# Kernel optimization log

Measured on AMD Instinct MI355X. Metric: run time of the kernel, lower is better.

Reference implementation:

```python
import jax, jax.numpy as jnp
import numpy as np

N_NODES = 50000
N_EDGES = 1600000
N_HEAD = 4
F_OUT = 128


def setup_inputs() -> dict:
    key = jax.random.key(0)
    k1, k2, k3, k4 = jax.random.split(key, 4)
    x = jax.random.normal(k1, (N_NODES, F_OUT), dtype=jnp.float32)
    # diag weight [H,1,F]; small scale like xavier on a diag-ish param
    w = jax.random.normal(k2, (N_HEAD, 1, F_OUT), dtype=jnp.float32) * 0.1
    # a_src_dst init: uniform(-stdv, stdv), stdv = 1/sqrt(2*f_out)
    stdv = 1.0 / np.sqrt(2 * F_OUT)
    a = jax.random.uniform(k3, (N_HEAD, 2 * F_OUT, 1), dtype=jnp.float32, minval=-stdv, maxval=stdv)
    edge_index = jax.random.randint(k4, (2, N_EDGES), 0, N_NODES, dtype=jnp.int64)
    return {"x": x, "w": w, "a": a, "edge_index": edge_index}


def reference(x, w, a, edge_index):
    # x: [N,F], w: [H,1,F] (diag), a: [H,2F,1], edge_index: [2,E]
    H, F = w.shape[0], w.shape[-1]
    N = x.shape[0]
    src = edge_index[0]  # row indices (aggregation targets)
    dst = edge_index[1]
    h = x[None, :, :] * w  # [H,N,F]  (diag: elementwise scale per head)
    # split cat(h_src,h_dst)@a into two per-node projections (same math as concat+matmul)
    a_src = a[:, :F, 0]  # [H,F]
    a_dst = a[:, F:, 0]  # [H,F]
    s_src = jnp.einsum('hnf,hf->hn', h, a_src)  # [H,N]
    s_dst = jnp.einsum('hnf,hf->hn', h, a_dst)  # [H,N]
    score = s_src[:, src] + s_dst[:, dst]  # [H,E]
    edge_e = jnp.exp(-jax.nn.leaky_relu(score, negative_slope=0.2))  # [H,E]
    outs = []
    for i in range(H):  # small fixed head loop keeps peak memory at one head's messages
        rowsum = jax.ops.segment_sum(edge_e[i], src, num_segments=N)  # [N]
        msg = edge_e[i][:, None] * h[i][dst]  # [E,F]
        agg = jax.ops.segment_sum(msg, src, num_segments=N)  # [N,F]
        outs.append(agg / rowsum[:, None])
    return jnp.stack(outs, axis=0)  # [H,N,F]
```

## Files before the change

kernel.cpp:

```cpp
#include <hip/hip_runtime.h>

#define N_NODES 50000
#define N_EDGES 1600000
#define N_HEAD 4
#define F_OUT 128
#define CAP 96
#define NPS 512
#define K1 98
#define SCAP 17408
#define NPG 32
#define GROUPS 1563
#define EPB 2048
#define P1_BLOCKS ((N_EDGES + EPB - 1) / EPB)
#define SCORE_BLOCKS ((N_NODES * 64 + 255) / 256)
#define FUSED_BLOCKS (P1_BLOCKS + SCORE_BLOCKS)

__global__ void __launch_bounds__(256) prep_kernel(
    const float* __restrict__ x, const float* __restrict__ w,
    const float* __restrict__ a, float4* __restrict__ s_src4,
    float4* __restrict__ s_dst4,
    const int* __restrict__ src, const int* __restrict__ dst,
    int* __restrict__ gc, unsigned int* __restrict__ region) {
  __shared__ int hist[K1], cur[K1], lstart[K1], gpos[K1];
  __shared__ unsigned int staging[EPB];
  const int tid = threadIdx.x;

  if (blockIdx.x >= P1_BLOCKS) {
    int bid = blockIdx.x - P1_BLOCKS;
    if (bid == 0 && tid == 0) {
      s_dst4[N_NODES] = make_float4(INFINITY, INFINITY, INFINITY, INFINITY);
    }
    int wv = (bid * 256 + tid) >> 6;
    int lane = tid & 63;
    if (wv >= N_NODES) return;
    float xv0 = x[wv * F_OUT + lane];
    float xv1 = x[wv * F_OUT + 64 + lane];
    float ps[N_HEAD], pd[N_HEAD];
#pragma unroll
    for (int h = 0; h < N_HEAD; ++h) {
      float w0 = w[h * F_OUT + lane];
      float w1 = w[h * F_OUT + 64 + lane];
      float as0 = a[h * 2 * F_OUT + lane];
      float as1 = a[h * 2 * F_OUT + 64 + lane];
      float ad0 = a[h * 2 * F_OUT + F_OUT + lane];
      float ad1 = a[h * 2 * F_OUT + F_OUT + 64 + lane];
      ps[h] = xv0 * w0 * as0 + xv1 * w1 * as1;
      pd[h] = xv0 * w0 * ad0 + xv1 * w1 * ad1;
    }
#pragma unroll
    for (int off = 32; off > 0; off >>= 1) {
#pragma unroll
      for (int h = 0; h < N_HEAD; ++h) {
        ps[h] += __shfl_xor(ps[h], off, 64);
        pd[h] += __shfl_xor(pd[h], off, 64);
      }
    }
    if (lane == 0) {
      s_src4[wv] = make_float4(ps[0], ps[1], ps[2], ps[3]);
      s_dst4[wv] = make_float4(pd[0], pd[1], pd[2], pd[3]);
    }
    return;
  }

  const int base = blockIdx.x * EPB;
  int vc = N_EDGES - base;
  if (vc > EPB) vc = EPB;

  unsigned int pk[EPB / 256];
#pragma unroll
  for (int k = 0; k < EPB / 256; ++k) {
    int i = k * 256 + tid;
    if (i < vc) {
      unsigned int s = (unsigned int)src[base + i];
      unsigned int d = (unsigned int)dst[base + i];
      pk[k] = (s << 16) | d;
    } else {
      pk[k] = 0xffffffffu;
    }
  }
  if (tid < K1) { hist[tid] = 0; cur[tid] = 0; }
  __syncthreads();
#pragma unroll
  for (int k = 0; k < EPB / 256; ++k)
    if (pk[k] != 0xffffffffu) atomicAdd(&hist[pk[k] >> 25], 1);
  __syncthreads();
  if (tid < 64) {
    int carry = 0;
    for (int b0 = 0; b0 < K1; b0 += 64) {
      int idx = b0 + tid;
      int h = (idx < K1) ? hist[idx] : 0;
      int v = h;
#pragma unroll
      for (int off = 1; off < 64; off <<= 1) {
        int t = __shfl_up(v, off, 64);
        if (tid >= off) v += t;
      }
      if (idx < K1) {
        lstart[idx] = carry + v - h;
        gpos[idx] = atomicAdd(&gc[idx], h);
      }
      carry += __shfl(v, 63, 64);
    }
  }
  __syncthreads();
#pragma unroll
  for (int k = 0; k < EPB / 256; ++k) {
    if (pk[k] != 0xffffffffu) {
      int b = pk[k] >> 25;
      int pos = lstart[b] + atomicAdd(&cur[b], 1);
      staging[pos] = pk[k];
    }
  }
  __syncthreads();
  for (int i = tid; i < vc; i += 256) {
    unsigned int v = staging[i];
    int b = v >> 25;
    int off = gpos[b] + (i - lstart[b]);
    if (off < SCAP) region[(size_t)b * SCAP + off] = v;
  }
}


#define SCAN_PROC(v)                                                       \
  {                                                                        \
    unsigned int s_ = (v) >> 16;                                           \
    if ((s_ >> 5) == gtag) {                                               \
      int l_ = s_ & 31;                                                    \
      int p_ = atomicAdd(&ncnt[l_], 1);                                    \
      if (p_ < CAP) nbkt[l_][p_] = (int)((v) & 0xffffu);                   \
    }                                                                      \
  }

__global__ void __launch_bounds__(256, 6) agg_kernel(
    const float* __restrict__ x, const float* __restrict__ w,
    const float4* __restrict__ s_src4, const float4* __restrict__ s_dst4,
    const int* __restrict__ gc, const unsigned int* __restrict__ region,
    float* __restrict__ out) {
  __shared__ int ncnt[NPG];
  __shared__ int nbkt[NPG][CAP];
  const int tid = threadIdx.x;
  const int g = blockIdx.x;
  const int sb = g >> 4;
  int c = gc[sb];
  if (c > SCAP) c = SCAP;
  if (tid < NPG) ncnt[tid] = 0;
  __syncthreads();

  const unsigned int* reg = region + (size_t)sb * SCAP;
  const unsigned int gtag = (unsigned int)g;
  {
    const uint4* reg4 = (const uint4*)reg;
    int c4 = c >> 2;
    for (int i = tid; i < c4; i += 256) {
      uint4 v = reg4[i];
      SCAN_PROC(v.x); SCAN_PROC(v.y); SCAN_PROC(v.z); SCAN_PROC(v.w);
    }
    for (int i = (c4 << 2) + tid; i < c; i += 256) {
      unsigned int v = reg[i];
      SCAN_PROC(v);
    }
  }
  __syncthreads();

  const int ws = tid >> 6, lane = tid & 63;
  const int half = lane >> 5;
  const int sl = lane & 31;
  const float4* x4 = (const float4*)x;

  const float4* w4 = (const float4*)w;
  const float4 wA = w4[(half ? 1 : 0) * 32 + sl];
  const float4 wB = w4[(half ? 3 : 2) * 32 + sl];

  float4 ss = s_src4[g * NPG + ws];

  for (int l = ws; l < NPG; l += 4) {
    int n = g * NPG + l;
    if (n >= N_NODES) break;
    int nn = n + 4;
    if (nn > N_NODES - 1) nn = N_NODES - 1;
    float4 ss_next = s_src4[nn];

    int m = ncnt[l];
    m = (m < CAP) ? m : CAP;
    int m_pad = (m + 7) & ~7;
    if (lane < m_pad - m) nbkt[l][m + lane] = N_NODES;

    float4 acc0 = {0.f, 0.f, 0.f, 0.f}, acc1 = {0.f, 0.f, 0.f, 0.f};
    float4 acc2 = {0.f, 0.f, 0.f, 0.f}, acc3 = {0.f, 0.f, 0.f, 0.f};
    float p0 = 0.f, p1 = 0.f, p2 = 0.f, p3 = 0.f;

    for (int t = 0; t < m_pad; t += 8) {
      int dd[4];
      float4 sd[4], xv[4];
#pragma unroll
      for (int q = 0; q < 4; ++q) dd[q] = nbkt[l][t + 2 * q + half];
#pragma unroll
      for (int q = 0; q < 4; ++q) sd[q] = s_dst4[dd[q]];
#pragma unroll
      for (int q = 0; q < 4; ++q) {
        int dx = dd[q] < N_NODES - 1 ? dd[q] : N_NODES - 1;
        xv[q] = x4[(size_t)dx * 32 + sl];
      }
#pragma unroll
      for (int q = 0; q < 4; ++q) {
        float s0 = ss.x + sd[q].x, s1 = ss.y + sd[q].y;
        float s2 = ss.z + sd[q].z, s3 = ss.w + sd[q].w;
        float e0 = __expf(-fmaxf(s0, 0.2f * s0));
        float e1 = __expf(-fmaxf(s1, 0.2f * s1));
        float e2 = __expf(-fmaxf(s2, 0.2f * s2));
        float e3 = __expf(-fmaxf(s3, 0.2f * s3));
        p0 += e0; p1 += e1; p2 += e2; p3 += e3;
        acc0.x = fmaf(e0, xv[q].x, acc0.x); acc0.y = fmaf(e0, xv[q].y, acc0.y);
        acc0.z = fmaf(e0, xv[q].z, acc0.z); acc0.w = fmaf(e0, xv[q].w, acc0.w);
        acc1.x = fmaf(e1, xv[q].x, acc1.x); acc1.y = fmaf(e1, xv[q].y, acc1.y);
        acc1.z = fmaf(e1, xv[q].z, acc1.z); acc1.w = fmaf(e1, xv[q].w, acc1.w);
        acc2.x = fmaf(e2, xv[q].x, acc2.x); acc2.y = fmaf(e2, xv[q].y, acc2.y);
        acc2.z = fmaf(e2, xv[q].z, acc2.z); acc2.w = fmaf(e2, xv[q].w, acc2.w);
        acc3.x = fmaf(e3, xv[q].x, acc3.x); acc3.y = fmaf(e3, xv[q].y, acc3.y);
        acc3.z = fmaf(e3, xv[q].z, acc3.z); acc3.w = fmaf(e3, xv[q].w, acc3.w);
      }
    }

    p0 += __shfl_xor(p0, 32, 64);
    p1 += __shfl_xor(p1, 32, 64);
    p2 += __shfl_xor(p2, 32, 64);
    p3 += __shfl_xor(p3, 32, 64);

    acc0.x += __shfl_xor(acc0.x, 32, 64); acc0.y += __shfl_xor(acc0.y, 32, 64);
    acc0.z += __shfl_xor(acc0.z, 32, 64); acc0.w += __shfl_xor(acc0.w, 32, 64);
    acc1.x += __shfl_xor(acc1.x, 32, 64); acc1.y += __shfl_xor(acc1.y, 32, 64);
    acc1.z += __shfl_xor(acc1.z, 32, 64); acc1.w += __shfl_xor(acc1.w, 32, 64);
    acc2.x += __shfl_xor(acc2.x, 32, 64); acc2.y += __shfl_xor(acc2.y, 32, 64);
    acc2.z += __shfl_xor(acc2.z, 32, 64); acc2.w += __shfl_xor(acc2.w, 32, 64);
    acc3.x += __shfl_xor(acc3.x, 32, 64); acc3.y += __shfl_xor(acc3.y, 32, 64);
    acc3.z += __shfl_xor(acc3.z, 32, 64); acc3.w += __shfl_xor(acc3.w, 32, 64);

    float r0 = 1.f / p0, r1 = 1.f / p1, r2 = 1.f / p2, r3 = 1.f / p3;

    float4 aA = half ? acc1 : acc0;
    float4 aB = half ? acc3 : acc2;
    float rA = half ? r1 : r0;
    float rB = half ? r3 : r2;
    float4 o;
    o.x = wA.x * aA.x * rA; o.y = wA.y * aA.y * rA;
    o.z = wA.z * aA.z * rA; o.w = wA.w * aA.w * rA;
    *(float4*)(out + ((size_t)half * N_NODES + n) * F_OUT + 4 * sl) = o;
    o.x = wB.x * aB.x * rB; o.y = wB.y * aB.y * rB;
    o.z = wB.z * aB.z * rB; o.w = wB.w * aB.w * rB;
    *(float4*)(out + ((size_t)(2 + half) * N_NODES + n) * F_OUT + 4 * sl) = o;

    ss = ss_next;
  }
}

extern "C" void kernel_launch(void* const* d_in, const int* in_sizes, int n_in,
                              void* d_out, int out_size, void* d_ws, size_t ws_size,
                              hipStream_t stream) {
  const float* x = (const float*)d_in[0];
  const float* w = (const float*)d_in[1];
  const float* a = (const float*)d_in[2];
  const int* ei = (const int*)d_in[3];
  const int* src = ei;
  const int* dst = ei + N_EDGES;
  float* out = (float*)d_out;

  char* p = (char*)d_ws;
  float4* s_src4 = (float4*)p;      p += (size_t)(N_NODES + 1) * 16;
  float4* s_dst4 = (float4*)p;      p += (size_t)(N_NODES + 1) * 16;
  int* gc = (int*)p;                p += 4096;
  unsigned int* region = (unsigned int*)p;
  p += (size_t)K1 * SCAP * 4;

  hipMemsetAsync(gc, 0, 4096, stream);

  prep_kernel<<<FUSED_BLOCKS, 256, 0, stream>>>(x, w, a, s_src4, s_dst4,
                                                src, dst, gc, region);
  agg_kernel<<<GROUPS, 256, 0, stream>>>(x, w, s_src4, s_dst4, gc, region, out);
}
```

Baseline: 335.7 us.

## Precompute per-edge attention weights into double-buffered LDS and software-pipeline gathers

Edge weights for all four heads are now computed once per edge, one lane per edge, and stored in a per-wave LDS double buffer. Before, every lane in a half-wave recomputed the same s_dst load and exponentials. The weights and row sums for the next node are computed while the current node's feature gathers run, and the x-row gather loop is software-pipelined with ping-pong register sets. The row sum is reduced with a full-wave shuffle tree, and the launch-bounds occupancy hint drops from 6 to 4 blocks to leave room for the extra registers and LDS.

```diff
diff --git a/kernel.cpp b/kernel.cpp
--- a/kernel.cpp
+++ b/kernel.cpp
@@ -121,6 +121,27 @@
 }
 
 
+#define EDGE_FMA(W, X)                                                     \
+  acc0.x = fmaf(W.x, X.x, acc0.x); acc0.y = fmaf(W.x, X.y, acc0.y);        \
+  acc0.z = fmaf(W.x, X.z, acc0.z); acc0.w = fmaf(W.x, X.w, acc0.w);        \
+  acc1.x = fmaf(W.y, X.x, acc1.x); acc1.y = fmaf(W.y, X.y, acc1.y);        \
+  acc1.z = fmaf(W.y, X.z, acc1.z); acc1.w = fmaf(W.y, X.w, acc1.w);        \
+  acc2.x = fmaf(W.z, X.x, acc2.x); acc2.y = fmaf(W.z, X.y, acc2.y);        \
+  acc2.z = fmaf(W.z, X.z, acc2.z); acc2.w = fmaf(W.z, X.w, acc2.w);        \
+  acc3.x = fmaf(W.w, X.x, acc3.x); acc3.y = fmaf(W.w, X.y, acc3.y);        \
+  acc3.z = fmaf(W.w, X.z, acc3.z); acc3.w = fmaf(W.w, X.w, acc3.w);
+
+#define LOADB(t, D0, D1, D2, D3, X0, X1, X2, X3)                           \
+  D0 = nbkt[l][(t) + half];     D1 = nbkt[l][(t) + 2 + half];              \
+  D2 = nbkt[l][(t) + 4 + half]; D3 = nbkt[l][(t) + 6 + half];              \
+  X0 = x4[(size_t)D0 * 32 + sl]; X1 = x4[(size_t)D1 * 32 + sl];            \
+  X2 = x4[(size_t)D2 * 32 + sl]; X3 = x4[(size_t)D3 * 32 + sl];
+
+#define FMA8(t, X0, X1, X2, X3)                                            \
+  { const float4* wp = &lds_w[ws][cur][(t) + half];                        \
+    float4 w0_ = wp[0], w1_ = wp[2], w2_ = wp[4], w3_ = wp[6];             \
+    EDGE_FMA(w0_, X0) EDGE_FMA(w1_, X1) EDGE_FMA(w2_, X2) EDGE_FMA(w3_, X3) }
+
 #define SCAN_PROC(v)                                                       \
   {                                                                        \
     unsigned int s_ = (v) >> 16;                                           \
@@ -131,13 +152,14 @@
     }                                                                      \
   }
 
-__global__ void __launch_bounds__(256, 6) agg_kernel(
+__global__ void __launch_bounds__(256, 4) agg_kernel(
     const float* __restrict__ x, const float* __restrict__ w,
     const float4* __restrict__ s_src4, const float4* __restrict__ s_dst4,
     const int* __restrict__ gc, const unsigned int* __restrict__ region,
     float* __restrict__ out) {
   __shared__ int ncnt[NPG];
   __shared__ int nbkt[NPG][CAP];
+  __shared__ float4 lds_w[4][2][CAP];
   const int tid = threadIdx.x;
   const int g = blockIdx.x;
   const int sb = g >> 4;
@@ -171,60 +193,117 @@
   const float4 wA = w4[(half ? 1 : 0) * 32 + sl];
   const float4 wB = w4[(half ? 3 : 2) * 32 + sl];
 
-  float4 ss = s_src4[g * NPG + ws];
+  int mp;
+  float pl0, pl1, pl2, pl3;
+  {
+    int l = ws;
+    int m = ncnt[l];
+    m = (m < CAP) ? m : CAP;
+    mp = (m + 7) & ~7;
+    if (lane < mp - m) nbkt[l][m + lane] = 0;
+    int d = (lane < m) ? nbkt[l][lane] : N_NODES;
+    float4 sd = s_dst4[d];
+    float4 ssc = s_src4[g * NPG + l];
+    float s0 = ssc.x + sd.x, s1 = ssc.y + sd.y;
+    float s2 = ssc.z + sd.z, s3 = ssc.w + sd.w;
+    float e0 = __expf(-fmaxf(s0, 0.2f * s0));
+    float e1 = __expf(-fmaxf(s1, 0.2f * s1));
+    float e2 = __expf(-fmaxf(s2, 0.2f * s2));
+    float e3 = __expf(-fmaxf(s3, 0.2f * s3));
+    lds_w[ws][0][lane] = make_float4(e0, e1, e2, e3);
+    pl0 = e0; pl1 = e1; pl2 = e2; pl3 = e3;
+    if (m > 64) {
+      for (int j = 64 + lane; j < m; j += 64) {
+        int dj = nbkt[l][j];
+        float4 sdj = s_dst4[dj];
+        float t0 = ssc.x + sdj.x, t1 = ssc.y + sdj.y;
+        float t2 = ssc.z + sdj.z, t3 = ssc.w + sdj.w;
+        float f0 = __expf(-fmaxf(t0, 0.2f * t0));
+        float f1 = __expf(-fmaxf(t1, 0.2f * t1));
+        float f2 = __expf(-fmaxf(t2, 0.2f * t2));
+        float f3 = __expf(-fmaxf(t3, 0.2f * t3));
+        lds_w[ws][0][j] = make_float4(f0, f1, f2, f3);
+        pl0 += f0; pl1 += f1; pl2 += f2; pl3 += f3;
+      }
+      if (lane < mp - m) lds_w[ws][0][m + lane] = make_float4(0.f, 0.f, 0.f, 0.f);
+    }
+  }
+  int cur = 0;
 
   for (int l = ws; l < NPG; l += 4) {
     int n = g * NPG + l;
     if (n >= N_NODES) break;
-    int nn = n + 4;
-    if (nn > N_NODES - 1) nn = N_NODES - 1;
-    float4 ss_next = s_src4[nn];
-
-    int m = ncnt[l];
-    m = (m < CAP) ? m : CAP;
-    int m_pad = (m + 7) & ~7;
-    if (lane < m_pad - m) nbkt[l][m + lane] = N_NODES;
+    const int lnext = l + 4;
+    const int nnext = g * NPG + lnext;
+    const bool have_next = (lnext < NPG) && (nnext < N_NODES);
+
+    int mn = 0, mpn = 0;
+    float4 sdn, ssn;
+    if (have_next) {
+      mn = ncnt[lnext];
+      mn = (mn < CAP) ? mn : CAP;
+      mpn = (mn + 7) & ~7;
+      if (lane < mpn - mn) nbkt[lnext][mn + lane] = 0;
+      int dn = (lane < mn) ? nbkt[lnext][lane] : N_NODES;
+      sdn = s_dst4[dn];
+      ssn = s_src4[nnext];
+    }
 
     float4 acc0 = {0.f, 0.f, 0.f, 0.f}, acc1 = {0.f, 0.f, 0.f, 0.f};
     float4 acc2 = {0.f, 0.f, 0.f, 0.f}, acc3 = {0.f, 0.f, 0.f, 0.f};
-    float p0 = 0.f, p1 = 0.f, p2 = 0.f, p3 = 0.f;
-
-    for (int t = 0; t < m_pad; t += 8) {
-      int dd[4];
-      float4 sd[4], xv[4];
-#pragma unroll
-      for (int q = 0; q < 4; ++q) dd[q] = nbkt[l][t + 2 * q + half];
-#pragma unroll
-      for (int q = 0; q < 4; ++q) sd[q] = s_dst4[dd[q]];
-#pragma unroll
-      for (int q = 0; q < 4; ++q) {
-        int dx = dd[q] < N_NODES - 1 ? dd[q] : N_NODES - 1;
-        xv[q] = x4[(size_t)dx * 32 + sl];
-      }
-#pragma unroll
-      for (int q = 0; q < 4; ++q) {
-        float s0 = ss.x + sd[q].x, s1 = ss.y + sd[q].y;
-        float s2 = ss.z + sd[q].z, s3 = ss.w + sd[q].w;
-        float e0 = __expf(-fmaxf(s0, 0.2f * s0));
-        float e1 = __expf(-fmaxf(s1, 0.2f * s1));
-        float e2 = __expf(-fmaxf(s2, 0.2f * s2));
-        float e3 = __expf(-fmaxf(s3, 0.2f * s3));
-        p0 += e0; p1 += e1; p2 += e2; p3 += e3;
-        acc0.x = fmaf(e0, xv[q].x, acc0.x); acc0.y = fmaf(e0, xv[q].y, acc0.y);
-        acc0.z = fmaf(e0, xv[q].z, acc0.z); acc0.w = fmaf(e0, xv[q].w, acc0.w);
-        acc1.x = fmaf(e1, xv[q].x, acc1.x); acc1.y = fmaf(e1, xv[q].y, acc1.y);
-        acc1.z = fmaf(e1, xv[q].z, acc1.z); acc1.w = fmaf(e1, xv[q].w, acc1.w);
-        acc2.x = fmaf(e2, xv[q].x, acc2.x); acc2.y = fmaf(e2, xv[q].y, acc2.y);
-        acc2.z = fmaf(e2, xv[q].z, acc2.z); acc2.w = fmaf(e2, xv[q].w, acc2.w);
-        acc3.x = fmaf(e3, xv[q].x, acc3.x); acc3.y = fmaf(e3, xv[q].y, acc3.y);
-        acc3.z = fmaf(e3, xv[q].z, acc3.z); acc3.w = fmaf(e3, xv[q].w, acc3.w);
-      }
-    }
-
-    p0 += __shfl_xor(p0, 32, 64);
-    p1 += __shfl_xor(p1, 32, 64);
-    p2 += __shfl_xor(p2, 32, 64);
-    p3 += __shfl_xor(p3, 32, 64);
+    if (mp > 0) {
+      int da0, da1, da2, da3, db0, db1, db2, db3;
+      float4 xa0, xa1, xa2, xa3, xb0, xb1, xb2, xb3;
+      LOADB(0, da0, da1, da2, da3, xa0, xa1, xa2, xa3)
+      int tB = 0;
+      for (;;) {
+        if (tB + 8 >= mp) { FMA8(tB, xa0, xa1, xa2, xa3) break; }
+        LOADB(tB + 8, db0, db1, db2, db3, xb0, xb1, xb2, xb3)
+        FMA8(tB, xa0, xa1, xa2, xa3)
+        tB += 8;
+        if (tB + 8 >= mp) { FMA8(tB, xb0, xb1, xb2, xb3) break; }
+        LOADB(tB + 8, da0, da1, da2, da3, xa0, xa1, xa2, xa3)
+        FMA8(tB, xb0, xb1, xb2, xb3)
+        tB += 8;
+      }
+    }
+
+    float pn0 = 0.f, pn1 = 0.f, pn2 = 0.f, pn3 = 0.f;
+    if (have_next) {
+      float s0 = ssn.x + sdn.x, s1 = ssn.y + sdn.y;
+      float s2 = ssn.z + sdn.z, s3 = ssn.w + sdn.w;
+      float e0 = __expf(-fmaxf(s0, 0.2f * s0));
+      float e1 = __expf(-fmaxf(s1, 0.2f * s1));
+      float e2 = __expf(-fmaxf(s2, 0.2f * s2));
+      float e3 = __expf(-fmaxf(s3, 0.2f * s3));
+      lds_w[ws][cur ^ 1][lane] = make_float4(e0, e1, e2, e3);
+      pn0 = e0; pn1 = e1; pn2 = e2; pn3 = e3;
+      if (mn > 64) {
+        for (int j = 64 + lane; j < mn; j += 64) {
+          int dj = nbkt[lnext][j];
+          float4 sdj = s_dst4[dj];
+          float t0 = ssn.x + sdj.x, t1 = ssn.y + sdj.y;
+          float t2 = ssn.z + sdj.z, t3 = ssn.w + sdj.w;
+          float f0 = __expf(-fmaxf(t0, 0.2f * t0));
+          float f1 = __expf(-fmaxf(t1, 0.2f * t1));
+          float f2 = __expf(-fmaxf(t2, 0.2f * t2));
+          float f3 = __expf(-fmaxf(t3, 0.2f * t3));
+          lds_w[ws][cur ^ 1][j] = make_float4(f0, f1, f2, f3);
+          pn0 += f0; pn1 += f1; pn2 += f2; pn3 += f3;
+        }
+        if (lane < mpn - mn)
+          lds_w[ws][cur ^ 1][mn + lane] = make_float4(0.f, 0.f, 0.f, 0.f);
+      }
+    }
+
+#pragma unroll
+    for (int off = 32; off > 0; off >>= 1) {
+      pl0 += __shfl_xor(pl0, off, 64);
+      pl1 += __shfl_xor(pl1, off, 64);
+      pl2 += __shfl_xor(pl2, off, 64);
+      pl3 += __shfl_xor(pl3, off, 64);
+    }
+    float r0 = 1.f / pl0, r1 = 1.f / pl1, r2 = 1.f / pl2, r3 = 1.f / pl3;
 
     acc0.x += __shfl_xor(acc0.x, 32, 64); acc0.y += __shfl_xor(acc0.y, 32, 64);
     acc0.z += __shfl_xor(acc0.z, 32, 64); acc0.w += __shfl_xor(acc0.w, 32, 64);
@@ -234,8 +313,6 @@
     acc2.z += __shfl_xor(acc2.z, 32, 64); acc2.w += __shfl_xor(acc2.w, 32, 64);
     acc3.x += __shfl_xor(acc3.x, 32, 64); acc3.y += __shfl_xor(acc3.y, 32, 64);
     acc3.z += __shfl_xor(acc3.z, 32, 64); acc3.w += __shfl_xor(acc3.w, 32, 64);
-
-    float r0 = 1.f / p0, r1 = 1.f / p1, r2 = 1.f / p2, r3 = 1.f / p3;
 
     float4 aA = half ? acc1 : acc0;
     float4 aB = half ? acc3 : acc2;
@@ -249,7 +326,9 @@
     o.z = wB.z * aB.z * rB; o.w = wB.w * aB.w * rB;
     *(float4*)(out + ((size_t)(2 + half) * N_NODES + n) * F_OUT + 4 * sl) = o;
 
-    ss = ss_next;
+    pl0 = pn0; pl1 = pn1; pl2 = pn2; pl3 = pn3;
+    mp = mpn;
+    cur ^= 1;
   }
 }
 
```

Measured after the change: 328.6 us. -2.1%, faster.
